# Optimization experiments

Measured on AMD Instinct MI355X. Metric: run time of the kernel, lower is better.

## Reference

```python
import jax, jax.numpy as jnp
import numpy as np

B, C, H, W = 16, 128, 64, 64
K, P = 16, 3  # number of basis functions, spline degree


def _open_uniform_knots(K, p):
    # [low x (p+1), interior, high x (p+1)], total K+p+1 knots on [-1, 1]
    n_interior = K - p - 1
    interior = np.linspace(-1.0, 1.0, n_interior + 2)[1:-1] if n_interior > 0 else np.zeros((0,))
    knots = np.concatenate([np.full(p + 1, -1.0), interior, np.full(p + 1, 1.0)])
    return jnp.asarray(knots, dtype=jnp.float32)


def _bspline_basis(x, knots, p):
    # Cox-de Boor recursion. x: (...,), knots: (K+p+1,) -> basis (..., K)
    Kn = knots.shape[0] - p - 1
    L = Kn + p
    xe = x[..., None]
    t0, t1 = knots[:-1], knots[1:]
    N = ((xe >= t0) & (xe < t1)).astype(x.dtype)
    # right-closed at the last knot: basis = e_{L-1}
    last_onehot = jnp.zeros((L,), x.dtype).at[L - 1].set(1.0)
    N = jnp.where(xe == knots[-1], last_onehot, N)
    for r in range(1, p + 1):
        Lr = Kn + p - (r - 1)
        left_den = knots[r:r + Lr - 1] - knots[:Lr - 1]
        right_den = knots[r + 1:r + Lr] - knots[1:Lr]
        safe_ld = jnp.where(left_den != 0, left_den, 1.0)
        safe_rd = jnp.where(right_den != 0, right_den, 1.0)
        left = jnp.where(left_den != 0, (xe - knots[:Lr - 1]) / safe_ld * N[..., :Lr - 1], 0.0)
        right = jnp.where(right_den != 0, (knots[r + 1:r + Lr] - xe) / safe_rd * N[..., 1:Lr], 0.0)
        N = left + right
    return N  # (..., K)


def setup_inputs() -> dict:
    key = jax.random.key(0)
    ks = jax.random.split(key, 6)
    x = jax.random.normal(ks[0], (B, C, H, W), dtype=jnp.float32)
    a = 1.0 + 0.1 * jax.random.normal(ks[1], (C,), dtype=jnp.float32)
    b = 0.1 * jax.random.normal(ks[2], (C,), dtype=jnp.float32)
    alpha = 0.1 * jax.random.normal(ks[3], (C, K), dtype=jnp.float32)
    id_gain = 1.0 + 0.1 * jax.random.normal(ks[4], (C,), dtype=jnp.float32)
    bias = 0.1 * jax.random.normal(ks[5], (C,), dtype=jnp.float32)
    return {"x": x, "a": a, "b": b, "alpha": alpha, "id_gain": id_gain, "bias": bias}


def reference(x, a, b, alpha, id_gain, bias):
    knots = _open_uniform_knots(K, P)
    ac = a[None, :, None, None]
    bc = b[None, :, None, None]
    x_aff = jnp.clip(x * ac + bc, -1.5, 1.5)
    basis = _bspline_basis(x_aff, knots, P)            # (B,C,H,W,K)
    spline_val = jnp.einsum('bchwk,ck->bchw', basis, alpha)
    return id_gain[None, :, None, None] * x + spline_val + bias[None, :, None, None]
```

## Files before the change

### kernel.cpp

```cpp
#include <hip/hip_runtime.h>


__device__ __forceinline__ float knot_val(int m) {
    const float h = 2.0f / 13.0f;
    return fminf(fmaxf(fmaf((float)(m - 3), h, -1.0f), -1.0f), 1.0f);
}

__device__ __forceinline__ void basis_span(float t, int j,
                                           float& N0, float& N1, float& N2, float& N3) {
    const float invh = 6.5f;
    auto invD3 = [&](int m) -> float {
        return (m == 1 || m == 15) ? invh
             : ((m == 2 || m == 14) ? 0.5f * invh : invh * (1.0f / 3.0f));
    };
    const float left1  = t - knot_val(j);
    const float right1 = knot_val(j + 1) - t;
    const float left2  = t - knot_val(j - 1);
    const float right2 = knot_val(j + 2) - t;
    const float left3  = t - knot_val(j - 2);
    const float right3 = knot_val(j + 3) - t;
    const float invD2_jm1 = (j == 3)  ? invh : 0.5f * invh;
    const float invD2_j   = (j == 15) ? invh : 0.5f * invh;

    float temp, saved;
    temp = invh;
    N0 = right1 * temp;
    N1 = left1 * temp;
    temp  = N0 * invD2_jm1;
    N0    = right1 * temp;
    saved = left2 * temp;
    temp  = N1 * invD2_j;
    N1    = saved + right2 * temp;
    N2    = left1 * temp;
    temp  = N0 * invD3(j - 2);
    N0    = right1 * temp;
    saved = left3 * temp;
    temp  = N1 * invD3(j - 1);
    N1    = saved + right2 * temp;
    saved = left2 * temp;
    temp  = N2 * invD3(j);
    N2    = saved + right3 * temp;
    N3    = left1 * temp;
}

__global__ __launch_bounds__(256) void kan_coeff_kernel(
    const float* __restrict__ alpha,
    float4* __restrict__ coef)
{
    int tid = blockIdx.x * blockDim.x + threadIdx.x;
    if (tid >= 128 * 13) return;
    const int c = tid / 13;
    const int s = tid - c * 13;
    const int j = s + 3;
    const float h = 2.0f / 13.0f;

    const float a0 = alpha[(c << 4) + s];
    const float a1 = alpha[(c << 4) + s + 1];
    const float a2 = alpha[(c << 4) + s + 2];
    const float a3 = alpha[(c << 4) + s + 3];

    float y[4];
#pragma unroll
    for (int k = 0; k < 4; ++k) {
        const float u = (float)k * (1.0f / 3.0f);
        const float t = fmaf((float)s + u, h, -1.0f);
        float N0, N1, N2, N3;
        basis_span(t, j, N0, N1, N2, N3);
        y[k] = N0 * a0 + N1 * a1 + N2 * a2 + N3 * a3;
    }
    const float d1 = y[1] - y[0];
    const float d2 = y[2] - 2.0f * y[1] + y[0];
    const float d3 = y[3] - 3.0f * y[2] + 3.0f * y[1] - y[0];
    float4 cf;
    cf.x = y[0];
    cf.y = 3.0f * d1 - 1.5f * d2 + d3;
    cf.z = 4.5f * d2 - 4.5f * d3;
    cf.w = 4.5f * d3;
    coef[tid] = cf;
}

__global__ __launch_bounds__(256) void kan_spline_kernel(
    const float* __restrict__ x,
    const float* __restrict__ a,
    const float* __restrict__ b,
    const float* __restrict__ gain,
    const float* __restrict__ bias,
    const float4* __restrict__ coef,
    float* __restrict__ out,
    int n4)
{
    int i = blockIdx.x * blockDim.x + threadIdx.x;
    if (i >= n4) return;

    const int c = (i >> 10) & 127;
    const float ac  = a[c];
    const float bc  = b[c];
    const float gc  = gain[c];
    const float bic = bias[c];
    const float4* __restrict__ Ct = coef + c * 13;

    float4 xv = reinterpret_cast<const float4*>(x)[i];
    float4 ov;

#pragma unroll
    for (int e = 0; e < 4; ++e) {
        const float xs = (&xv.x)[e];
        const float t = fminf(fmaxf(fmaf(xs, ac, bc), -1.5f), 1.5f);
        const float f = fmaf(t, 6.5f, 6.5f);
        int s = (int)f;
        s = min(max(s, 0), 12);
        const float u = f - (float)s;
        const float4 cf = Ct[s];
        float p = fmaf(fmaf(fmaf(cf.w, u, cf.z), u, cf.y), u, cf.x);
        p = (t >= -1.0f && t < 1.0f) ? p : 0.0f;
        (&ov.x)[e] = fmaf(gc, xs, p + bic);
    }

    reinterpret_cast<float4*>(out)[i] = ov;
}

extern "C" void kernel_launch(void* const* d_in, const int* in_sizes, int n_in,
                              void* d_out, int out_size, void* d_ws, size_t ws_size,
                              hipStream_t stream) {
    const float* x     = (const float*)d_in[0];
    const float* a     = (const float*)d_in[1];
    const float* b     = (const float*)d_in[2];
    const float* alpha = (const float*)d_in[3];
    const float* gain  = (const float*)d_in[4];
    const float* bias  = (const float*)d_in[5];
    float* out = (float*)d_out;
    float4* coef = (float4*)d_ws;

    kan_coeff_kernel<<<(128 * 13 + 255) / 256, 256, 0, stream>>>(alpha, coef);

    const int n4 = out_size / 4;
    const int block = 256;
    const int grid = (n4 + block - 1) / block;
    kan_spline_kernel<<<grid, block, 0, stream>>>(x, a, b, gain, bias, coef, out, n4);
}
```

Before: 95.05 us.

## Fuse spline coefficient precompute into main kernel via shared memory

Removes the separate coefficient kernel launch and has each block compute its channel's 13 cubic segment coefficients into shared memory, then evaluate from LDS instead of global gathers. The x load is issued before the coefficient work so it overlaps with that computation. This saves one launch and the dependency between the two kernels. In exchange, every block redundantly recomputes the coefficients and adds a __syncthreads barrier, and the block-to-channel mapping now assumes 4 blocks per channel.

```diff
diff --git a/kernel.cpp b/kernel.cpp
--- a/kernel.cpp
+++ b/kernel.cpp
@@ -43,65 +43,65 @@
     N3    = left1 * temp;
 }
 
-__global__ __launch_bounds__(256) void kan_coeff_kernel(
-    const float* __restrict__ alpha,
-    float4* __restrict__ coef)
-{
-    int tid = blockIdx.x * blockDim.x + threadIdx.x;
-    if (tid >= 128 * 13) return;
-    const int c = tid / 13;
-    const int s = tid - c * 13;
-    const int j = s + 3;
-    const float h = 2.0f / 13.0f;
-
-    const float a0 = alpha[(c << 4) + s];
-    const float a1 = alpha[(c << 4) + s + 1];
-    const float a2 = alpha[(c << 4) + s + 2];
-    const float a3 = alpha[(c << 4) + s + 3];
-
-    float y[4];
-#pragma unroll
-    for (int k = 0; k < 4; ++k) {
-        const float u = (float)k * (1.0f / 3.0f);
-        const float t = fmaf((float)s + u, h, -1.0f);
-        float N0, N1, N2, N3;
-        basis_span(t, j, N0, N1, N2, N3);
-        y[k] = N0 * a0 + N1 * a1 + N2 * a2 + N3 * a3;
-    }
-    const float d1 = y[1] - y[0];
-    const float d2 = y[2] - 2.0f * y[1] + y[0];
-    const float d3 = y[3] - 3.0f * y[2] + 3.0f * y[1] - y[0];
-    float4 cf;
-    cf.x = y[0];
-    cf.y = 3.0f * d1 - 1.5f * d2 + d3;
-    cf.z = 4.5f * d2 - 4.5f * d3;
-    cf.w = 4.5f * d3;
-    coef[tid] = cf;
-}
-
-__global__ __launch_bounds__(256) void kan_spline_kernel(
+__global__ __launch_bounds__(256) void kan_fused_kernel(
     const float* __restrict__ x,
     const float* __restrict__ a,
     const float* __restrict__ b,
+    const float* __restrict__ alpha,
     const float* __restrict__ gain,
     const float* __restrict__ bias,
-    const float4* __restrict__ coef,
     float* __restrict__ out,
     int n4)
 {
-    int i = blockIdx.x * blockDim.x + threadIdx.x;
-    if (i >= n4) return;
+    __shared__ float4 Csh[13];
 
-    const int c = (i >> 10) & 127;
+    const int i = blockIdx.x * blockDim.x + threadIdx.x;
+    const bool active = (i < n4);
+    const int c = (blockIdx.x >> 2) & 127;
+
+    float4 xv = make_float4(0.0f, 0.0f, 0.0f, 0.0f);
+    if (active) xv = reinterpret_cast<const float4*>(x)[i];
+
+    if (threadIdx.x < 13) {
+        const int s = (int)threadIdx.x;
+        const int j = s + 3;
+        const float h = 2.0f / 13.0f;
+
+        const float a0 = alpha[(c << 4) + s];
+        const float a1 = alpha[(c << 4) + s + 1];
+        const float a2 = alpha[(c << 4) + s + 2];
+        const float a3 = alpha[(c << 4) + s + 3];
+
+        float y[4];
+#pragma unroll
+        for (int k = 0; k < 4; ++k) {
+            const float u = (float)k * (1.0f / 3.0f);
+            const float t = fmaf((float)s + u, h, -1.0f);
+            float N0, N1, N2, N3;
+            basis_span(t, j, N0, N1, N2, N3);
+            y[k] = N0 * a0 + N1 * a1 + N2 * a2 + N3 * a3;
+        }
+        const float d1 = y[1] - y[0];
+        const float d2 = y[2] - 2.0f * y[1] + y[0];
+        const float d3 = y[3] - 3.0f * y[2] + 3.0f * y[1] - y[0];
+        float4 cf;
+        cf.x = y[0];
+        cf.y = 3.0f * d1 - 1.5f * d2 + d3;
+        cf.z = 4.5f * d2 - 4.5f * d3;
+        cf.w = 4.5f * d3;
+        Csh[s] = cf;
+    }
+
     const float ac  = a[c];
     const float bc  = b[c];
     const float gc  = gain[c];
     const float bic = bias[c];
-    const float4* __restrict__ Ct = coef + c * 13;
 
-    float4 xv = reinterpret_cast<const float4*>(x)[i];
+    __syncthreads();
+
+    if (!active) return;
+
     float4 ov;
-
 #pragma unroll
     for (int e = 0; e < 4; ++e) {
         const float xs = (&xv.x)[e];
@@ -110,7 +110,7 @@
         int s = (int)f;
         s = min(max(s, 0), 12);
         const float u = f - (float)s;
-        const float4 cf = Ct[s];
+        const float4 cf = Csh[s];
         float p = fmaf(fmaf(fmaf(cf.w, u, cf.z), u, cf.y), u, cf.x);
         p = (t >= -1.0f && t < 1.0f) ? p : 0.0f;
         (&ov.x)[e] = fmaf(gc, xs, p + bic);
@@ -129,12 +129,10 @@
     const float* gain  = (const float*)d_in[4];
     const float* bias  = (const float*)d_in[5];
     float* out = (float*)d_out;
-    float4* coef = (float4*)d_ws;
-
-    kan_coeff_kernel<<<(128 * 13 + 255) / 256, 256, 0, stream>>>(alpha, coef);
+    (void)d_ws; (void)ws_size;
 
     const int n4 = out_size / 4;
     const int block = 256;
     const int grid = (n4 + block - 1) / block;
-    kan_spline_kernel<<<grid, block, 0, stream>>>(x, a, b, gain, bias, coef, out, n4);
+    kan_fused_kernel<<<grid, block, 0, stream>>>(x, a, b, alpha, gain, bias, out, n4);
 }
```

New measurement: 92.63 us. 1.03x faster.
